# Performance work log

Hardware: AMD Instinct MI355X
Metric: run time of the kernel (lower is better)

Reference implementation:

```python
import jax, jax.numpy as jnp
import numpy as np

B, D, LC, LQ = 64, 128, 1000, 100


def setup_inputs() -> dict:
    key = jax.random.key(0)
    kc, kq, kw = jax.random.split(key, 3)
    C = jax.random.normal(kc, (B, D, LC), dtype=jnp.float32)
    Q = jax.random.normal(kq, (B, D, LQ), dtype=jnp.float32)
    # xavier_normal over fan_in=1 rows x fan_out=3D cols per [1, 3D] slice
    std = float(np.sqrt(2.0 / (1 + 3 * D)))
    W = jax.random.normal(kw, (B * LC, 1, 3 * D), dtype=jnp.float32) * std
    return {"C": C, "Q": Q, "W": W}


def reference(C, Q, W):
    # C: [B, D, Lc], Q: [B, D, Lq], W: [B*Lc, 1, 3D]
    Ct = jnp.transpose(C, (0, 2, 1))  # [B, Lc, D]
    Qt = jnp.transpose(Q, (0, 2, 1))  # [B, Lq, D]
    Wr = W.reshape(B, LC, 3 * D)
    w1, w2, w3 = Wr[:, :, :D], Wr[:, :, D:2 * D], Wr[:, :, 2 * D:]
    # Trilinear similarity decomposed into three terms (concat order: [Qi, C, Q*C])
    S = (
        jnp.einsum("bid,bjd->bij", w1, Qt)
        + jnp.sum(w2 * Ct, axis=-1, keepdims=True)
        + jnp.einsum("bid,bjd->bij", w3 * Ct, Qt)
    )  # [B, Lc, Lq]
    S1 = jax.nn.softmax(S, axis=2)  # over query positions
    S2 = jax.nn.softmax(S, axis=1)  # over context positions
    A = jnp.einsum("bij,bjd->bid", S1, Qt)  # context-to-query [B, Lc, D]
    Bm = jnp.einsum("bik,bkd->bid", jnp.einsum("bij,bkj->bik", S1, S2), Ct)
    out = jnp.concatenate([Ct, A, Ct * A, Ct * Bm], axis=2)  # [B, Lc, 4D]
    return jnp.transpose(out, (0, 2, 1))  # [B, 4D, Lc]
```

## Files before the change

kernel.cpp:

```cpp
#include <hip/hip_runtime.h>
#include <cstddef>

#define B_  64
#define D_  128
#define LC_ 1000
#define LQ_ 100
#define SP  104
#define JP  128

__global__ __launch_bounds__(256) void k_transpose(const float* __restrict__ C,
                                                   float* __restrict__ Ct){
  __shared__ float t[32][33];
  int b  = blockIdx.z;
  int i0 = blockIdx.x * 32;
  int d0 = blockIdx.y * 32;
  int tx = threadIdx.x, ty = threadIdx.y;
  const float* Cb  = C  + (size_t)b * D_ * LC_;
  float*       Ctb = Ct + (size_t)b * LC_ * D_;
#pragma unroll
  for(int k=0;k<4;k++){
    int d = d0 + ty + 8*k;
    int i = i0 + tx;
    t[ty+8*k][tx] = (i < LC_) ? Cb[(size_t)d*LC_ + i] : 0.f;
  }
  __syncthreads();
#pragma unroll
  for(int k=0;k<4;k++){
    int i = i0 + ty + 8*k;
    int d = d0 + tx;
    if(i < LC_) Ctb[(size_t)i*D_ + d] = t[tx][ty+8*k];
  }
}

__global__ __launch_bounds__(256) void k_transposeQ(const float* __restrict__ Q,
                                                    float* __restrict__ Qt){
  __shared__ float t[32][33];
  int b  = blockIdx.z;
  int j0 = blockIdx.x * 32;
  int d0 = blockIdx.y * 32;
  int tx = threadIdx.x, ty = threadIdx.y;
  const float* Qb  = Q  + (size_t)b * D_ * LQ_;
  float*       Qtb = Qt + (size_t)b * LQ_ * D_;
#pragma unroll
  for(int k=0;k<4;k++){
    int d = d0 + ty + 8*k;
    int j = j0 + tx;
    t[ty+8*k][tx] = (j < LQ_) ? Qb[(size_t)d*LQ_ + j] : 0.f;
  }
  __syncthreads();
#pragma unroll
  for(int k=0;k<4;k++){
    int j = j0 + ty + 8*k;
    int d = d0 + tx;
    if(j < LQ_) Qtb[(size_t)j*D_ + d] = t[tx][ty+8*k];
  }
}

__global__ __launch_bounds__(256) void k_S(const float* __restrict__ Q,
                                           const float* __restrict__ W,
                                           const float* __restrict__ Ct,
                                           float* __restrict__ S){
  __shared__ float Qs[32][132];
  __shared__ float Vs[64][33];
  __shared__ float t2s[64];
  int b   = blockIdx.y;
  int i0  = blockIdx.x * 64;
  int tid = threadIdx.x;
  const float* Wb  = W  + (size_t)b * LC_ * 384;
  const float* Ctb = Ct + (size_t)b * LC_ * D_;
  const float* Qb  = Q  + (size_t)b * D_ * LQ_;

  {
    int g = tid >> 5, l = tid & 31;
    for(int rep=0; rep<8; rep++){
      int il = rep*8 + g;
      int i  = i0 + il;
      float s = 0.f;
      if(i < LC_){
        const float* wrow  = Wb  + (size_t)i*384 + 128;
        const float* ctrow = Ctb + (size_t)i*D_;
#pragma unroll
        for(int k=0;k<4;k++){ int d = l + 32*k; s += wrow[d]*ctrow[d]; }
      }
#pragma unroll
      for(int m=16;m>0;m>>=1) s += __shfl_xor(s, m, 64);
      if(l==0) t2s[il] = s;
    }
  }

  int jt = tid & 15;
  int ti = tid >> 4;
  float acc[4][8] = {};

  for(int c=0;c<4;c++){
    int dc0 = c*32;
    __syncthreads();
    for(int idx=tid; idx<32*128; idx+=256){
      int dc = idx >> 7, j = idx & 127;
      Qs[dc][j] = (j < LQ_) ? Qb[(size_t)(dc0+dc)*LQ_ + j] : 0.f;
    }
    for(int idx=tid; idx<64*32; idx+=256){
      int il = idx >> 5, dc = idx & 31;
      int i = i0 + il;
      float v = 0.f;
      if(i < LC_){
        const float* wrow = Wb + (size_t)i*384;
        float ct = Ctb[(size_t)i*D_ + dc0+dc];
        v = wrow[dc0+dc] + wrow[256+dc0+dc]*ct;
      }
      Vs[il][dc] = v;
    }
    __syncthreads();
#pragma unroll 4
    for(int dc=0; dc<32; dc++){
      float v[4];
#pragma unroll
      for(int ii=0; ii<4; ii++) v[ii] = Vs[ti*4+ii][dc];
      float4 q0 = *(const float4*)&Qs[dc][jt*8];
      float4 q1 = *(const float4*)&Qs[dc][jt*8+4];
      float q[8] = {q0.x,q0.y,q0.z,q0.w,q1.x,q1.y,q1.z,q1.w};
#pragma unroll
      for(int ii=0; ii<4; ii++)
#pragma unroll
        for(int jj=0; jj<8; jj++) acc[ii][jj] += v[ii]*q[jj];
    }
  }
  float* Sb = S + (size_t)b * LC_ * SP;
#pragma unroll
  for(int ii=0; ii<4; ii++){
    int il = ti*4+ii;
    int i  = i0 + il;
    if(i < LC_){
      float t2v = t2s[il];
      float4 o0, o1;
      o0.x=acc[ii][0]+t2v; o0.y=acc[ii][1]+t2v; o0.z=acc[ii][2]+t2v; o0.w=acc[ii][3]+t2v;
      o1.x=acc[ii][4]+t2v; o1.y=acc[ii][5]+t2v; o1.z=acc[ii][6]+t2v; o1.w=acc[ii][7]+t2v;
      if(jt*8   < SP) *(float4*)&Sb[(size_t)i*SP + jt*8    ] = o0;
      if(jt*8+4 < SP) *(float4*)&Sb[(size_t)i*SP + jt*8 + 4] = o1;
    }
  }
}

#define NIC 8
__global__ __launch_bounds__(256) void k_colstats1(const float* __restrict__ S,
                                                   float* __restrict__ pm,
                                                   float* __restrict__ ps){
  __shared__ float lm[8][128], lsum[8][128];
  int b = blockIdx.x, ic = blockIdx.y;
  int tid = threadIdx.x;
  int jt = tid & 31, h = tid >> 5;
  int j0 = jt*4;
  int ni = min(16, 125 - h*16);
  const float* Sb = S + (size_t)b * LC_ * SP;
  float m[4] = {-1e30f,-1e30f,-1e30f,-1e30f}, s[4] = {0.f,0.f,0.f,0.f};
  if(jt < 26){
    for(int r=0;r<ni;r++){
      int i = ic*125 + h*16 + r;
      float4 x = *(const float4*)&Sb[(size_t)i*SP + j0];
      float xv[4] = {x.x,x.y,x.z,x.w};
#pragma unroll
      for(int k=0;k<4;k++){
        if(xv[k] > m[k]){ s[k] = s[k]*__expf(m[k]-xv[k]) + 1.f; m[k] = xv[k]; }
        else              s[k] += __expf(xv[k]-m[k]);
      }
    }
  }
#pragma unroll
  for(int k=0;k<4;k++){
    int j = j0+k;
    if(j < 128){ lm[h][j] = m[k]; lsum[h][j] = s[k]; }
  }
  __syncthreads();
  if(tid < 128){
    float mm = -1e30f, ss = 0.f;
#pragma unroll
    for(int hh=0; hh<8; hh++){
      float m2 = lm[hh][tid], s2 = lsum[hh][tid];
      if(m2 > mm){ ss = ss*__expf(mm-m2) + s2; mm = m2; }
      else         ss += s2*__expf(m2-mm);
    }
    pm[((size_t)b*NIC + ic)*128 + tid] = mm;
    ps[((size_t)b*NIC + ic)*128 + tid] = ss;
  }
}

__global__ __launch_bounds__(128) void k_colstats2(const float* __restrict__ pm,
                                                   const float* __restrict__ ps,
                                                   float* __restrict__ cm,
                                                   float* __restrict__ cs){
  int b = blockIdx.x, j = threadIdx.x;
  float mm = -1e30f, ss = 0.f;
#pragma unroll
  for(int ic=0; ic<NIC; ic++){
    float m2 = pm[((size_t)b*NIC + ic)*128 + j];
    float s2 = ps[((size_t)b*NIC + ic)*128 + j];
    if(m2 > mm){ ss = ss*__expf(mm-m2) + s2; mm = m2; }
    else         ss += s2*__expf(m2-mm);
  }
  cm[b*JP + j] = mm;
  cs[b*JP + j] = (ss == 0.f) ? 1.f : ss;
}

#define MJQ 25
__global__ __launch_bounds__(256) void k_Mj(const float* __restrict__ S,
                                            const float* __restrict__ Ct,
                                            const float* __restrict__ cm_,
                                            const float* __restrict__ cs_,
                                            float* __restrict__ M){
  __shared__ float Es[32][32];
  __shared__ float Cs[32][132];
  __shared__ float cml[32], icsl[32];
  int b  = blockIdx.x;
  int jq = blockIdx.y;
  int j0 = jq * MJQ;
  int tid = threadIdx.x;
  if(tid < 32){
    int j = j0 + tid;
    cml[tid]  = (tid < MJQ && j < LQ_) ? cm_[b*JP + j] : 0.f;
    icsl[tid] = (tid < MJQ && j < LQ_) ? 1.f/cs_[b*JP + j] : 0.f;
  }
  __syncthreads();
  int dt = tid & 31;
  int jt = tid >> 5;
  float acc[4][4] = {};
  const float* Sb  = S  + (size_t)b * LC_ * SP + j0;
  const float* Ctb = Ct + (size_t)b * LC_ * D_;

  for(int i0=0; i0<LC_; i0+=32){
    int rem = min(32, LC_ - i0);
    __syncthreads();
    for(int idx=tid; idx<32*32; idx+=256){
      int ii = idx >> 5, jl = idx & 31;
      float e = 0.f;
      if(ii < rem && jl < MJQ && (j0+jl) < LQ_)
        e = __expf(Sb[(size_t)(i0+ii)*SP + jl] - cml[jl]);
      Es[ii][jl] = e;
    }
    for(int idx=tid; idx<32*32; idx+=256){
      int ii = idx >> 5, f = idx & 31;
      float4 v = make_float4(0.f,0.f,0.f,0.f);
      if(ii < rem) v = *(const float4*)&Ctb[(size_t)(i0+ii)*D_ + f*4];
      *(float4*)&Cs[ii][f*4] = v;
    }
    __syncthreads();
#pragma unroll 8
    for(int ii=0; ii<32; ii++){
      float4 e4 = *(const float4*)&Es[ii][jt*4];
      float4 c4 = *(const float4*)&Cs[ii][dt*4];
      float e[4] = {e4.x,e4.y,e4.z,e4.w};
      float c[4] = {c4.x,c4.y,c4.z,c4.w};
#pragma unroll
      for(int jj=0; jj<4; jj++)
#pragma unroll
        for(int dd=0; dd<4; dd++) acc[jj][dd] += e[jj]*c[dd];
    }
  }
  float* Mb = M + (size_t)b * JP * D_;
#pragma unroll
  for(int jj=0; jj<4; jj++){
    int jl = jt*4 + jj;
    if(jl < MJQ && (j0+jl) < LQ_){
      float ics = icsl[jl];
      float4 o;
      o.x = acc[jj][0]*ics; o.y = acc[jj][1]*ics;
      o.z = acc[jj][2]*ics; o.w = acc[jj][3]*ics;
      *(float4*)&Mb[(size_t)(j0+jl)*D_ + dt*4] = o;
    }
  }
}

__global__ __launch_bounds__(256) void k_final(const float* __restrict__ S,
                                               const float* __restrict__ Qt,
                                               const float* __restrict__ M,
                                               const float* __restrict__ C,
                                               float* __restrict__ out){
  __shared__ float lds[10880];
  float* S1s = lds;
  float* Qc  = lds + 6656;
  float* Mc  = lds + 8768;
  float* At  = lds;
  int b   = blockIdx.y;
  int i0  = blockIdx.x * 64;
  int tid = threadIdx.x;
  const float* Sb  = S  + (size_t)b * LC_ * SP;
  const float* Qtb = Qt + (size_t)b * LQ_ * D_;
  const float* Mb  = M  + (size_t)b * JP * D_;

  for(int idx=tid; idx<64*26; idx+=256){
    int il = idx / 26, f = idx % 26;
    int i = i0 + il;
    float4 v = make_float4(0.f,0.f,0.f,0.f);
    if(i < LC_ && f < 25) v = *(const float4*)&Sb[(size_t)i*SP + f*4];
    *(float4*)&S1s[il*104 + f*4] = v;
  }
  __syncthreads();

  {
    int w = tid >> 6, l = tid & 63;
    for(int r=0; r<16; r++){
      int il = w*16 + r;
      float x0 = (2*l   < LQ_) ? S1s[il*104 + 2*l  ] : -1e30f;
      float x1 = (2*l+1 < LQ_) ? S1s[il*104 + 2*l+1] : -1e30f;
      float m = fmaxf(x0,x1);
#pragma unroll
      for(int mm=32;mm>0;mm>>=1) m = fmaxf(m, __shfl_xor(m, mm, 64));
      float e0 = (2*l   < LQ_) ? __expf(x0-m) : 0.f;
      float e1 = (2*l+1 < LQ_) ? __expf(x1-m) : 0.f;
      float s = e0+e1;
#pragma unroll
      for(int mm=32;mm>0;mm>>=1) s += __shfl_xor(s, mm, 64);
      float inv = 1.f/s;
      if(2*l   < LQ_) S1s[il*104 + 2*l  ] = e0*inv;
      if(2*l+1 < LQ_) S1s[il*104 + 2*l+1] = e1*inv;
    }
  }

  int dt = tid & 31;
  int it = tid >> 5;
  float A[8][4] = {}, Bm[8][4] = {};
  for(int j0=0; j0<LQ_; j0+=16){
    int nj = min(16, LQ_-j0);
    __syncthreads();
    for(int idx=tid; idx<nj*32; idx+=256){
      int jj = idx >> 5, f = idx & 31;
      *(float4*)&Qc[jj*132 + f*4] = *(const float4*)&Qtb[(size_t)(j0+jj)*D_ + f*4];
      *(float4*)&Mc[jj*132 + f*4] = *(const float4*)&Mb [(size_t)(j0+jj)*D_ + f*4];
    }
    __syncthreads();
    for(int jj4=0; jj4<nj; jj4+=4){
      float4 sv[8], qv[4], mv[4];
#pragma unroll
      for(int ii=0; ii<8; ii++) sv[ii] = *(const float4*)&S1s[(it*8+ii)*104 + j0+jj4];
#pragma unroll
      for(int jj=0; jj<4; jj++){
        qv[jj] = *(const float4*)&Qc[(jj4+jj)*132 + dt*4];
        mv[jj] = *(const float4*)&Mc[(jj4+jj)*132 + dt*4];
      }
#pragma unroll
      for(int ii=0; ii<8; ii++){
        float sf[4] = {sv[ii].x, sv[ii].y, sv[ii].z, sv[ii].w};
#pragma unroll
        for(int jj=0; jj<4; jj++){
          A[ii][0]  += sf[jj]*qv[jj].x; A[ii][1]  += sf[jj]*qv[jj].y;
          A[ii][2]  += sf[jj]*qv[jj].z; A[ii][3]  += sf[jj]*qv[jj].w;
          Bm[ii][0] += sf[jj]*mv[jj].x; Bm[ii][1] += sf[jj]*mv[jj].y;
          Bm[ii][2] += sf[jj]*mv[jj].z; Bm[ii][3] += sf[jj]*mv[jj].w;
        }
      }
    }
  }

  const float* Cb = C + (size_t)b * D_ * LC_;
  float* ob = out + (size_t)b * 512 * LC_;
  int il2 = tid & 63, dg = tid >> 6;
  int i = i0 + il2;

  __syncthreads();
#pragma unroll
  for(int ii=0; ii<8; ii++)
#pragma unroll
    for(int dd=0; dd<4; dd++) At[(it*8+ii)*133 + dt*4+dd] = A[ii][dd];
  __syncthreads();
  if(i < LC_){
    for(int dd2=0; dd2<32; dd2++){
      int d = dg*32 + dd2;
      float a = At[il2*133 + d];
      float c = Cb[(size_t)d*LC_ + i];
      ob[(size_t)d*LC_ + i]       = c;
      ob[(size_t)(128+d)*LC_ + i] = a;
      ob[(size_t)(256+d)*LC_ + i] = c*a;
    }
  }
  __syncthreads();
#pragma unroll
  for(int ii=0; ii<8; ii++)
#pragma unroll
    for(int dd=0; dd<4; dd++) At[(it*8+ii)*133 + dt*4+dd] = Bm[ii][dd];
  __syncthreads();
  if(i < LC_){
    for(int dd2=0; dd2<32; dd2++){
      int d = dg*32 + dd2;
      float bm = At[il2*133 + d];
      float c  = Cb[(size_t)d*LC_ + i];
      ob[(size_t)(384+d)*LC_ + i] = c*bm;
    }
  }
}

extern "C" void kernel_launch(void* const* d_in, const int* in_sizes, int n_in,
                              void* d_out, int out_size, void* d_ws, size_t ws_size,
                              hipStream_t stream){
  const float* C = (const float*)d_in[0];
  const float* Q = (const float*)d_in[1];
  const float* W = (const float*)d_in[2];
  float* out = (float*)d_out;
  float* ws  = (float*)d_ws;
  float* S  = ws;
  float* Ct = ws + 6656000;
  float* M  = ws + 14848000;
  float* Qt = ws + 15896576;
  float* pm = ws + 16715776;
  float* ps = ws + 16781312;
  float* cm = ws + 16846848;
  float* cs = ws + 16855040;

  k_transpose <<<dim3(32,4,64), dim3(32,8), 0, stream>>>(C, Ct);
  k_transposeQ<<<dim3(4,4,64),  dim3(32,8), 0, stream>>>(Q, Qt);
  k_S         <<<dim3(16,64),   256, 0, stream>>>(Q, W, Ct, S);
  k_colstats1 <<<dim3(64,NIC),  256, 0, stream>>>(S, pm, ps);
  k_colstats2 <<<64,            128, 0, stream>>>(pm, ps, cm, cs);
  k_Mj        <<<dim3(64,4),    256, 0, stream>>>(S, Ct, cm, cs, M);
  k_final     <<<dim3(16,64),   256, 0, stream>>>(S, Qt, M, C, out);
}
```

Before: 497.3 us.

## Split k_Mj context reduction across four thread groups with LDS merge

k_Mj now launches 1024 threads per block and splits the 1000-row context reduction into four 250-row slices, each handled by a 256-thread group with its own shared tiles. Partial accumulators are summed serially through a shared Macc buffer before group 0 scales and writes M. The aim is more parallelism per block, since the grid has only 256 blocks, cutting the long serial loop over context rows. In exchange it adds serialized LDS reductions, extra barriers and higher shared memory use per block.

```diff
diff --git a/kernel.cpp b/kernel.cpp
--- a/kernel.cpp
+++ b/kernel.cpp
@@ -202,51 +202,55 @@
 }
 
 #define MJQ 25
-__global__ __launch_bounds__(256) void k_Mj(const float* __restrict__ S,
-                                            const float* __restrict__ Ct,
-                                            const float* __restrict__ cm_,
-                                            const float* __restrict__ cs_,
-                                            float* __restrict__ M){
-  __shared__ float Es[32][32];
-  __shared__ float Cs[32][132];
+__global__ __launch_bounds__(1024) void k_Mj(const float* __restrict__ S,
+                                             const float* __restrict__ Ct,
+                                             const float* __restrict__ cm_,
+                                             const float* __restrict__ cs_,
+                                             float* __restrict__ M){
+  __shared__ float Es[4][16][32];
+  __shared__ float Cs[4][16][132];
+  __shared__ float Macc[25][132];
   __shared__ float cml[32], icsl[32];
   int b  = blockIdx.x;
   int jq = blockIdx.y;
   int j0 = jq * MJQ;
   int tid = threadIdx.x;
+  int grp = tid >> 8;
+  int t   = tid & 255;
   if(tid < 32){
     int j = j0 + tid;
     cml[tid]  = (tid < MJQ && j < LQ_) ? cm_[b*JP + j] : 0.f;
     icsl[tid] = (tid < MJQ && j < LQ_) ? 1.f/cs_[b*JP + j] : 0.f;
   }
   __syncthreads();
-  int dt = tid & 31;
-  int jt = tid >> 5;
+  int dt = t & 31;
+  int jt = t >> 5;
   float acc[4][4] = {};
   const float* Sb  = S  + (size_t)b * LC_ * SP + j0;
   const float* Ctb = Ct + (size_t)b * LC_ * D_;
-
-  for(int i0=0; i0<LC_; i0+=32){
-    int rem = min(32, LC_ - i0);
-    __syncthreads();
-    for(int idx=tid; idx<32*32; idx+=256){
+  int ibase = grp * 250;
+
+  for(int i0=0; i0<250; i0+=16){
+    int rem = min(16, 250 - i0);
+    __syncthreads();
+    for(int idx=t; idx<16*32; idx+=256){
       int ii = idx >> 5, jl = idx & 31;
       float e = 0.f;
-      if(ii < rem && jl < MJQ && (j0+jl) < LQ_)
-        e = __expf(Sb[(size_t)(i0+ii)*SP + jl] - cml[jl]);
-      Es[ii][jl] = e;
-    }
-    for(int idx=tid; idx<32*32; idx+=256){
+      if(ii < rem && jl < MJQ)
+        e = __expf(Sb[(size_t)(ibase+i0+ii)*SP + jl] - cml[jl]);
+      Es[grp][ii][jl] = e;
+    }
+    for(int idx=t; idx<16*32; idx+=256){
       int ii = idx >> 5, f = idx & 31;
       float4 v = make_float4(0.f,0.f,0.f,0.f);
-      if(ii < rem) v = *(const float4*)&Ctb[(size_t)(i0+ii)*D_ + f*4];
-      *(float4*)&Cs[ii][f*4] = v;
-    }
-    __syncthreads();
-#pragma unroll 8
-    for(int ii=0; ii<32; ii++){
-      float4 e4 = *(const float4*)&Es[ii][jt*4];
-      float4 c4 = *(const float4*)&Cs[ii][dt*4];
+      if(ii < rem) v = *(const float4*)&Ctb[(size_t)(ibase+i0+ii)*D_ + f*4];
+      *(float4*)&Cs[grp][ii][f*4] = v;
+    }
+    __syncthreads();
+#pragma unroll
+    for(int ii=0; ii<16; ii++){
+      float4 e4 = *(const float4*)&Es[grp][ii][jt*4];
+      float4 c4 = *(const float4*)&Cs[grp][ii][dt*4];
       float e[4] = {e4.x,e4.y,e4.z,e4.w};
       float c[4] = {c4.x,c4.y,c4.z,c4.w};
 #pragma unroll
@@ -255,16 +259,35 @@
         for(int dd=0; dd<4; dd++) acc[jj][dd] += e[jj]*c[dd];
     }
   }
-  float* Mb = M + (size_t)b * JP * D_;
-#pragma unroll
-  for(int jj=0; jj<4; jj++){
-    int jl = jt*4 + jj;
-    if(jl < MJQ && (j0+jl) < LQ_){
-      float ics = icsl[jl];
-      float4 o;
-      o.x = acc[jj][0]*ics; o.y = acc[jj][1]*ics;
-      o.z = acc[jj][2]*ics; o.w = acc[jj][3]*ics;
-      *(float4*)&Mb[(size_t)(j0+jl)*D_ + dt*4] = o;
+
+  for(int g=0; g<4; g++){
+    if(grp == g){
+#pragma unroll
+      for(int jj=0; jj<4; jj++){
+        int jl = jt*4 + jj;
+        if(jl < MJQ){
+#pragma unroll
+          for(int dd=0; dd<4; dd++){
+            if(g == 0) Macc[jl][dt*4+dd]  = acc[jj][dd];
+            else       Macc[jl][dt*4+dd] += acc[jj][dd];
+          }
+        }
+      }
+    }
+    __syncthreads();
+  }
+  if(grp == 0){
+    float* Mb = M + (size_t)b * JP * D_;
+#pragma unroll
+    for(int jj=0; jj<4; jj++){
+      int jl = jt*4 + jj;
+      if(jl < MJQ && (j0+jl) < LQ_){
+        float ics = icsl[jl];
+        float4 o;
+        o.x = Macc[jl][dt*4+0]*ics; o.y = Macc[jl][dt*4+1]*ics;
+        o.z = Macc[jl][dt*4+2]*ics; o.w = Macc[jl][dt*4+3]*ics;
+        *(float4*)&Mb[(size_t)(j0+jl)*D_ + dt*4] = o;
+      }
     }
   }
 }
@@ -409,6 +432,6 @@
   k_S         <<<dim3(16,64),   256, 0, stream>>>(Q, W, Ct, S);
   k_colstats1 <<<dim3(64,NIC),  256, 0, stream>>>(S, pm, ps);
   k_colstats2 <<<64,            128, 0, stream>>>(pm, ps, cm, cs);
-  k_Mj        <<<dim3(64,4),    256, 0, stream>>>(S, Ct, cm, cs, M);
+  k_Mj        <<<dim3(64,4),    1024, 0, stream>>>(S, Ct, cm, cs, M);
   k_final     <<<dim3(16,64),   256, 0, stream>>>(S, Qt, M, C, out);
 }
```

Result: faster. 421.1 us (-15.3%).
